# Optimization experiments

Hardware: AMD Instinct MI355X
Metric: run time of the kernel (lower is better)

Reference implementation:

```python
import jax, jax.numpy as jnp
import numpy as np

N_SRC0, N_DST0 = 100000, 20000   # block0: 100k src -> 20k dst
N_DST1 = 4096                    # block1: 20k src -> 4096 dst (seed nodes)


def setup_inputs() -> dict:
    key = jax.random.key(0)
    ks = jax.random.split(key, 8)
    E0, E1 = 640000, 131072
    return {
        "features": jax.random.normal(ks[0], (N_SRC0, 256), jnp.float32),
        "W1": jax.random.normal(ks[1], (256, 256), jnp.float32) * (1.0 / np.sqrt(256)),
        "b1": jnp.zeros((256,), jnp.float32),
        "W2": jax.random.normal(ks[2], (256, 128), jnp.float32) * (1.0 / np.sqrt(256)),
        "b2": jnp.zeros((128,), jnp.float32),
        "src0": jax.random.randint(ks[3], (E0,), 0, N_SRC0, jnp.int32),
        "dst0": jax.random.randint(ks[4], (E0,), 0, N_DST0, jnp.int32),
        "src1": jax.random.randint(ks[5], (E1,), 0, N_DST0, jnp.int32),
        "dst1": jax.random.randint(ks[6], (E1,), 0, N_DST1, jnp.int32),
    }


def _graph_conv(src, dst, n_dst, feat, W, b):
    # DGL GraphConv, norm='both': D_out^{-1/2} gather-sum D_in^{-1/2}, then WX+b.
    n_src = feat.shape[0]
    ones = jnp.ones(src.shape[0], feat.dtype)
    out_deg = jax.ops.segment_sum(ones, src, num_segments=n_src)
    norm_src = jnp.clip(out_deg, 1.0, None) ** -0.5          # [n_src]
    h = feat * norm_src[:, None]
    agg = jax.ops.segment_sum(h[src], dst, num_segments=n_dst)  # sparse SpMM
    in_deg = jax.ops.segment_sum(ones, dst, num_segments=n_dst)
    norm_dst = jnp.clip(in_deg, 1.0, None) ** -0.5           # [n_dst]
    return (agg * norm_dst[:, None]) @ W + b


def reference(features, W1, b1, W2, b2, src0, dst0, src1, dst1):
    x = jax.nn.relu(_graph_conv(src0, dst0, N_DST0, features, W1, b1))
    x = _graph_conv(src1, dst1, N_DST1, x, W2, b2)
    return x
```

## Files before the change

### kernel.cpp

```cpp
#include <hip/hip_runtime.h>
#include <hip/hip_bf16.h>

#define K_DIM 256
#define RSTRIDE 128
#define EPB 8192

#define G0_DB 625
#define G0_SB 256
#define G0_SW 392
#define G1_DB 128
#define G1_SB 64
#define G1_SW 313

#define NB_FIN (G0_DB + G1_DB + G0_SB + G1_SB)

typedef short bf16x8 __attribute__((ext_vector_type(8)));
typedef float f32x4 __attribute__((ext_vector_type(4)));

static __device__ __forceinline__ unsigned short f2bf(float x) {
    __hip_bfloat16 b = __float2bfloat16(x);
    return *reinterpret_cast<unsigned short*>(&b);
}
static __device__ __forceinline__ float bflo(unsigned int p) {
    return __uint_as_float(p << 16);
}
static __device__ __forceinline__ float bfhi(unsigned int p) {
    return __uint_as_float(p & 0xffff0000u);
}

static __device__ __forceinline__ void block_exscan(
        const int* __restrict__ hist, int* __restrict__ offs, int* __restrict__ tmp, int M) {
    const int tid = threadIdx.x;
    const int S = (M + 255) >> 8;
    const int base = tid * S;
    int sum = 0;
    for (int k = 0; k < S; ++k) {
        int idx = base + k;
        if (idx < M) sum += hist[idx];
    }
    tmp[tid] = sum;
    __syncthreads();
    for (int d = 1; d < 256; d <<= 1) {
        int v = tmp[tid];
        int u = (tid >= d) ? tmp[tid - d] : 0;
        __syncthreads();
        tmp[tid] = v + u;
        __syncthreads();
    }
    int run = (tid == 0) ? 0 : tmp[tid - 1];
    for (int k = 0; k < S; ++k) {
        int idx = base + k;
        if (idx < M) { offs[idx] = run; run += hist[idx]; }
    }
    __syncthreads();
}

struct SplitSh {
    int hist[640];
    int offs[640];
    int tmp[256];
    unsigned sorted[EPB];
};

template <int NDB, int NSB, int SW>
static __device__ __forceinline__ void split_sort(
        const int* __restrict__ src, const int* __restrict__ dst, int E, int chunk,
        int* __restrict__ cntD, int* __restrict__ offD,
        int* __restrict__ cntS, int* __restrict__ offS,
        unsigned* __restrict__ sortD, unsigned* __restrict__ sortS, SplitSh& sh) {
    const int tid = threadIdx.x;
    const int e0 = chunk * EPB;
    const int n = min(EPB, E - e0);
    for (int i = tid; i < NDB; i += 256) sh.hist[i] = 0;
    __syncthreads();
    for (int j = tid; j < n; j += 256) atomicAdd(&sh.hist[dst[e0 + j] >> 5], 1);
    __syncthreads();
    block_exscan(sh.hist, sh.offs, sh.tmp, NDB);
    for (int i = tid; i < NDB; i += 256) {
        cntD[chunk * NDB + i] = sh.hist[i];
        offD[chunk * NDB + i] = sh.offs[i];
    }
    __syncthreads();
    for (int j = tid; j < n; j += 256) {
        int d = dst[e0 + j];
        int s = src[e0 + j];
        int pos = atomicAdd(&sh.offs[d >> 5], 1);
        sh.sorted[pos] = ((unsigned)s << 5) | (unsigned)(d & 31);
    }
    __syncthreads();
    {
        unsigned* __restrict__ gout = sortD + (size_t)chunk * EPB;
        for (int j = tid; j < n; j += 256) gout[j] = sh.sorted[j];
    }
    __syncthreads();
    for (int i = tid; i < NSB; i += 256) sh.hist[i] = 0;
    __syncthreads();
    for (int j = tid; j < n; j += 256)
        atomicAdd(&sh.hist[(int)((unsigned)src[e0 + j] / SW)], 1);
    __syncthreads();
    block_exscan(sh.hist, sh.offs, sh.tmp, NSB);
    for (int i = tid; i < NSB; i += 256) {
        cntS[chunk * NSB + i] = sh.hist[i];
        offS[chunk * NSB + i] = sh.offs[i];
    }
    __syncthreads();
    for (int j = tid; j < n; j += 256) {
        unsigned s = (unsigned)src[e0 + j];
        int pos = atomicAdd(&sh.offs[s / SW], 1);
        sh.sorted[pos] = s;
    }
    __syncthreads();
    {
        unsigned* __restrict__ gout = sortS + (size_t)chunk * EPB;
        for (int j = tid; j < n; j += 256) gout[j] = sh.sorted[j];
    }
}

__global__ __launch_bounds__(256) void splitA_kernel(
        const int* __restrict__ src0, const int* __restrict__ dst0, int E0,
        const int* __restrict__ src1, const int* __restrict__ dst1, int E1,
        int* __restrict__ cntD0, int* __restrict__ offD0,
        int* __restrict__ cntS0, int* __restrict__ offS0,
        unsigned* __restrict__ sortD0, unsigned* __restrict__ sortS0,
        int* __restrict__ cntD1, int* __restrict__ offD1,
        int* __restrict__ cntS1, int* __restrict__ offS1,
        unsigned* __restrict__ sortD1, unsigned* __restrict__ sortS1,
        int nA0, int nA1,
        const float* __restrict__ feat, unsigned short* __restrict__ h, int total_f,
        int castBlocks,
        const float* __restrict__ W1, uint4* __restrict__ pw1,
        const float* __restrict__ W2, uint4* __restrict__ pw2) {
    __shared__ SplitSh sh;
    const int b = blockIdx.x;
    if (b < nA0) {
        split_sort<G0_DB, G0_SB, G0_SW>(src0, dst0, E0, b,
                                        cntD0, offD0, cntS0, offS0, sortD0, sortS0, sh);
    } else if (b < nA0 + nA1) {
        split_sort<G1_DB, G1_SB, G1_SW>(src1, dst1, E1, b - nA0,
                                        cntD1, offD1, cntS1, offS1, sortD1, sortS1, sh);
    } else if (b < nA0 + nA1 + castBlocks) {
        int idx = ((b - nA0 - nA1) * blockDim.x + threadIdx.x) * 8;
        if (idx >= total_f) return;
        const float4 v0 = *reinterpret_cast<const float4*>(feat + idx);
        const float4 v1 = *reinterpret_cast<const float4*>(feat + idx + 4);
        union { ushort4 u4[2]; uint4 u; } o;
        o.u4[0].x = f2bf(v0.x); o.u4[0].y = f2bf(v0.y);
        o.u4[0].z = f2bf(v0.z); o.u4[0].w = f2bf(v0.w);
        o.u4[1].x = f2bf(v1.x); o.u4[1].y = f2bf(v1.y);
        o.u4[1].z = f2bf(v1.z); o.u4[1].w = f2bf(v1.w);
        *reinterpret_cast<uint4*>(h + idx) = o.u;
    } else if (b < nA0 + nA1 + castBlocks + 32) {
        int idx = (b - nA0 - nA1 - castBlocks) * blockDim.x + threadIdx.x;
        int lane = idx & 63;
        int kt = (idx >> 6) & 7;
        int nt = idx >> 9;
        int n = nt * 16 + (lane & 15);
        int k = kt * 32 + (lane >> 4) * 8;
        union { unsigned short us[8]; uint4 u; } o;
#pragma unroll
        for (int j = 0; j < 8; ++j) o.us[j] = f2bf(W1[(size_t)(k + j) * 256 + n]);
        pw1[idx] = o.u;
    } else {
        int idx = (b - nA0 - nA1 - castBlocks - 32) * blockDim.x + threadIdx.x;
        int lane = idx & 63;
        int kt = (idx >> 6) & 7;
        int nt = idx >> 9;
        int n = nt * 16 + (lane & 15);
        int k = kt * 32 + (lane >> 4) * 8;
        union { unsigned short us[8]; uint4 u; } o;
#pragma unroll
        for (int j = 0; j < 8; ++j) o.us[j] = f2bf(W2[(size_t)(k + j) * 128 + n]);
        pw2[idx] = o.u;
    }
}

template <int NDB, int GT>
static __device__ __forceinline__ void fin_dst(
        const unsigned* __restrict__ sortD, const int* __restrict__ cntD,
        const int* __restrict__ offD, int nblk, int b,
        int* __restrict__ esrc, int* __restrict__ cnt, int* tile, int* rowc) {
    const int tid = threadIdx.x;
    if (tid < 32) rowc[tid] = 0;
    __syncthreads();
    for (int rr = tid / GT; rr < nblk; rr += 256 / GT) {
        const int c = cntD[rr * NDB + b];
        const int o = offD[rr * NDB + b];
        const unsigned* __restrict__ seg = sortD + (size_t)rr * EPB + o;
        for (int j = tid % GT; j < c; j += GT) {
            unsigned v = seg[j];
            int dloc = v & 31;
            int s = (int)(v >> 5);
            int slot = atomicAdd(&rowc[dloc], 1);
            if (slot < RSTRIDE) tile[(dloc << 7) + slot] = s;
        }
    }
    __syncthreads();
    int* __restrict__ gout = esrc + ((size_t)b << 12);
    for (int i = tid; i < 32 * RSTRIDE; i += 256) gout[i] = tile[i];
    if (tid < 32) cnt[b * 32 + tid] = rowc[tid];
}

template <int NSB, int SW, int GT>
static __device__ __forceinline__ void fin_src(
        const unsigned* __restrict__ sortS, const int* __restrict__ cntS,
        const int* __restrict__ offS, int nblk, int b, int NN,
        float* __restrict__ nv, int* hist) {
    const int tid = threadIdx.x;
    for (int i = tid; i < SW; i += 256) hist[i] = 0;
    __syncthreads();
    const int base = b * SW;
    for (int rr = tid / GT; rr < nblk; rr += 256 / GT) {
        const int c = cntS[rr * NSB + b];
        const int o = offS[rr * NSB + b];
        const unsigned* __restrict__ seg = sortS + (size_t)rr * EPB + o;
        for (int j = tid % GT; j < c; j += GT)
            atomicAdd(&hist[(int)seg[j] - base], 1);
    }
    __syncthreads();
    for (int i = tid; i < SW; i += 256) {
        int node = base + i;
        if (node < NN) nv[node] = rsqrtf((float)max(hist[i], 1));
    }
}

__global__ __launch_bounds__(256) void finalize_kernel(
        int nA0, int nA1,
        const unsigned* __restrict__ sortD0, const int* __restrict__ cntD0,
        const int* __restrict__ offD0, int* __restrict__ cnt0, int* __restrict__ esrc0,
        const unsigned* __restrict__ sortD1, const int* __restrict__ cntD1,
        const int* __restrict__ offD1, int* __restrict__ cnt1, int* __restrict__ esrc1,
        const unsigned* __restrict__ sortS0, const int* __restrict__ cntS0,
        const int* __restrict__ offS0, float* __restrict__ nv0,
        const unsigned* __restrict__ sortS1, const int* __restrict__ cntS1,
        const int* __restrict__ offS1, float* __restrict__ nv1) {
    __shared__ union {
        struct { int tile[32 * RSTRIDE]; int rowc[32]; } d;
        int hist[G0_SW];
    } sh;
    int b = blockIdx.x;
    if (b < G0_DB) {
        fin_dst<G0_DB, 2>(sortD0, cntD0, offD0, nA0, b, esrc0, cnt0, sh.d.tile, sh.d.rowc);
    } else if (b < G0_DB + G1_DB) {
        fin_dst<G1_DB, 16>(sortD1, cntD1, offD1, nA1, b - G0_DB, esrc1, cnt1,
                           sh.d.tile, sh.d.rowc);
    } else if (b < G0_DB + G1_DB + G0_SB) {
        fin_src<G0_SB, G0_SW, 2>(sortS0, cntS0, offS0, nA0, b - G0_DB - G1_DB,
                                 100000, nv0, sh.hist);
    } else {
        fin_src<G1_SB, G1_SW, 16>(sortS1, cntS1, offS1, nA1, b - G0_DB - G1_DB - G0_SB,
                                  20000, nv1, sh.hist);
    }
}

template <bool NORM>
static __device__ __forceinline__ void gather2_to_lds(
        const unsigned short* __restrict__ hfeat, const int* __restrict__ esrc,
        const int* __restrict__ cnt, const float* __restrict__ nv,
        int m0, int w, int lane, unsigned short (*Alds)[264]) {
#pragma unroll
    for (int k = 0; k < 2; ++k) {
        const int rloc = w * 2 + k;
        const int row = m0 + rloc;
        const int c = cnt[row];
        const int cend = min(c, RSTRIDE);
        const int* __restrict__ ep = esrc + ((size_t)row << 7);
        float a0 = 0.f, a1 = 0.f, a2 = 0.f, a3 = 0.f;
        int i = 0;
        for (; i + 7 < cend; i += 8) {
            int s[8];
            uint2 p[8];
            float nn[8];
#pragma unroll
            for (int u = 0; u < 8; ++u) s[u] = ep[i + u];
#pragma unroll
            for (int u = 0; u < 8; ++u)
                p[u] = *reinterpret_cast<const uint2*>(hfeat + (((size_t)s[u]) << 8) + lane * 4);
#pragma unroll
            for (int u = 0; u < 8; ++u)
                nn[u] = NORM ? nv[s[u]] : 1.0f;
#pragma unroll
            for (int u = 0; u < 8; ++u) {
                if (NORM) {
                    a0 = fmaf(bflo(p[u].x), nn[u], a0); a1 = fmaf(bfhi(p[u].x), nn[u], a1);
                    a2 = fmaf(bflo(p[u].y), nn[u], a2); a3 = fmaf(bfhi(p[u].y), nn[u], a3);
                } else {
                    a0 += bflo(p[u].x); a1 += bfhi(p[u].x);
                    a2 += bflo(p[u].y); a3 += bfhi(p[u].y);
                }
            }
        }
        for (; i < cend; ++i) {
            int s0 = ep[i];
            float n0 = NORM ? nv[s0] : 1.0f;
            const uint2 p0 = *reinterpret_cast<const uint2*>(hfeat + (((size_t)s0) << 8) + lane * 4);
            if (NORM) {
                a0 = fmaf(bflo(p0.x), n0, a0); a1 = fmaf(bfhi(p0.x), n0, a1);
                a2 = fmaf(bflo(p0.y), n0, a2); a3 = fmaf(bfhi(p0.y), n0, a3);
            } else {
                a0 += bflo(p0.x); a1 += bfhi(p0.x);
                a2 += bflo(p0.y); a3 += bfhi(p0.y);
            }
        }
        float nd = rsqrtf((float)max(c, 1));
        ushort4 o;
        o.x = f2bf(a0 * nd);
        o.y = f2bf(a1 * nd);
        o.z = f2bf(a2 * nd);
        o.w = f2bf(a3 * nd);
        *reinterpret_cast<ushort4*>(&Alds[rloc][lane * 4]) = o;
    }
}

__global__ __launch_bounds__(512, 8) void fused0_kernel(
        const unsigned short* __restrict__ hfeat, const int* __restrict__ esrc,
        const int* __restrict__ cnt, const float* __restrict__ nv0,
        const uint4* __restrict__ pW, const float* __restrict__ bias,
        const float* __restrict__ nv1, unsigned short* __restrict__ out) {
    __shared__ unsigned short Alds[16][264];
    const int m0 = blockIdx.x * 16;
    const int w = threadIdx.x >> 6;
    const int lane = threadIdx.x & 63;
    gather2_to_lds<true>(hfeat, esrc, cnt, nv0, m0, w, lane, Alds);
    __syncthreads();

    bf16x8 a[8];
    const unsigned short* ap = &Alds[lane & 15][(lane >> 4) * 8];
#pragma unroll
    for (int kt = 0; kt < 8; ++kt)
        a[kt] = *reinterpret_cast<const bf16x8*>(ap + kt * 32);

    const int rbase = m0 + (lane >> 4) * 4;
    float nsv[4];
#pragma unroll
    for (int r = 0; r < 4; ++r) nsv[r] = nv1[rbase + r];

#pragma unroll
    for (int nt = 0; nt < 2; ++nt) {
        const int n0 = w * 32 + nt * 16;
        f32x4 acc = {0.f, 0.f, 0.f, 0.f};
#pragma unroll
        for (int kt = 0; kt < 8; ++kt) {
            bf16x8 b = *reinterpret_cast<const bf16x8*>(&pW[((size_t)(n0 >> 4) * 8 + kt) * 64 + lane]);
            acc = __builtin_amdgcn_mfma_f32_16x16x32_bf16(a[kt], b, acc, 0, 0, 0);
        }
        const int col = n0 + (lane & 15);
        const float bv = bias[col];
#pragma unroll
        for (int r = 0; r < 4; ++r) {
            float v = fmaxf(acc[r] + bv, 0.0f) * nsv[r];
            out[(size_t)(rbase + r) * K_DIM + col] = f2bf(v);
        }
    }
}

__global__ __launch_bounds__(512, 8) void fused1_kernel(
        const unsigned short* __restrict__ xb, const int* __restrict__ esrc,
        const int* __restrict__ cnt,
        const uint4* __restrict__ pW, const float* __restrict__ bias,
        float* __restrict__ out) {
    __shared__ unsigned short Alds[16][264];
    const int m0 = blockIdx.x * 16;
    const int w = threadIdx.x >> 6;
    const int lane = threadIdx.x & 63;
    gather2_to_lds<false>(xb, esrc, cnt, nullptr, m0, w, lane, Alds);
    __syncthreads();

    bf16x8 a[8];
    const unsigned short* ap = &Alds[lane & 15][(lane >> 4) * 8];
#pragma unroll
    for (int kt = 0; kt < 8; ++kt)
        a[kt] = *reinterpret_cast<const bf16x8*>(ap + kt * 32);

    const int rbase = m0 + (lane >> 4) * 4;
    {
        const int n0 = w * 16;
        f32x4 acc = {0.f, 0.f, 0.f, 0.f};
#pragma unroll
        for (int kt = 0; kt < 8; ++kt) {
            bf16x8 b = *reinterpret_cast<const bf16x8*>(&pW[((size_t)(n0 >> 4) * 8 + kt) * 64 + lane]);
            acc = __builtin_amdgcn_mfma_f32_16x16x32_bf16(a[kt], b, acc, 0, 0, 0);
        }
        const int col = n0 + (lane & 15);
        const float bv = bias[col];
#pragma unroll
        for (int r = 0; r < 4; ++r)
            out[(size_t)(rbase + r) * 128 + col] = acc[r] + bv;
    }
}

__global__ __launch_bounds__(256) void gatherf_kernel(
        const float* __restrict__ feat, const int* __restrict__ esrc,
        const int* __restrict__ cnt, const int* __restrict__ od,
        float* __restrict__ outbuf, int n_dst) {
    int row = blockIdx.x * (blockDim.x >> 6) + (threadIdx.x >> 6);
    int lane = threadIdx.x & 63;
    if (row >= n_dst) return;
    const int c = cnt[row];
    const int cend = min(c, RSTRIDE);
    const int* __restrict__ ep = esrc + ((size_t)row << 7);
    float4 acc = {0.f, 0.f, 0.f, 0.f};
    for (int i = 0; i < cend; ++i) {
        int s0 = ep[i];
        float n0 = rsqrtf((float)max(od[s0], 1));
        const float4 v0 = *reinterpret_cast<const float4*>(feat + (((size_t)s0) << 8) + lane * 4);
        acc.x = fmaf(v0.x, n0, acc.x); acc.y = fmaf(v0.y, n0, acc.y);
        acc.z = fmaf(v0.z, n0, acc.z); acc.w = fmaf(v0.w, n0, acc.w);
    }
    float nd = rsqrtf((float)max(c, 1));
    float4 o = {acc.x * nd, acc.y * nd, acc.z * nd, acc.w * nd};
    *reinterpret_cast<float4*>(outbuf + (((size_t)row) << 8) + lane * 4) = o;
}

__global__ void edges_kernel(const int* __restrict__ src0, const int* __restrict__ dst0,
                             int* __restrict__ od0, int* __restrict__ cnt0,
                             int* __restrict__ esrc0, int E0,
                             const int* __restrict__ src1, const int* __restrict__ dst1,
                             int* __restrict__ od1, int* __restrict__ cnt1,
                             int* __restrict__ esrc1, int E1) {
    int i = blockIdx.x * blockDim.x + threadIdx.x;
    if (i < E0) {
        int s = src0[i];
        int d = dst0[i];
        atomicAdd(&od0[s], 1);
        int slot = atomicAdd(&cnt0[d], 1);
        if (slot < RSTRIDE) esrc0[(d << 7) + slot] = s;
    } else if (i < E0 + E1) {
        int e = i - E0;
        int s = src1[e];
        int d = dst1[e];
        atomicAdd(&od1[s], 1);
        int slot = atomicAdd(&cnt1[d], 1);
        if (slot < RSTRIDE) esrc1[(d << 7) + slot] = s;
    }
}

template <int ROWS, int NCOLS, bool RELU>
__global__ __launch_bounds__(NCOLS) void gemm_kernel(
        const float* __restrict__ A, const float* __restrict__ W,
        const float* __restrict__ bias, float* __restrict__ out, int M) {
    const int row0 = blockIdx.x * ROWS;
    const int c = threadIdx.x;
    const float* __restrict__ Ablk = A + (size_t)row0 * K_DIM;
    const float* __restrict__ Wc = W + c;

    float acc[ROWS];
#pragma unroll
    for (int r = 0; r < ROWS; ++r) acc[r] = 0.0f;

    float w0 = Wc[0];
    float w1 = Wc[NCOLS];
    float w2 = Wc[2 * NCOLS];
    float w3 = Wc[3 * NCOLS];

#pragma unroll 2
    for (int k = 0; k < K_DIM - 4; k += 4) {
        const float* p = Wc + (size_t)(k + 4) * NCOLS;
        float n0 = p[0];
        float n1 = p[NCOLS];
        float n2 = p[2 * NCOLS];
        float n3 = p[3 * NCOLS];
#pragma unroll
        for (int r = 0; r < ROWS; ++r) {
            const float4 a = *reinterpret_cast<const float4*>(Ablk + r * K_DIM + k);
            acc[r] = fmaf(a.x, w0, acc[r]);
            acc[r] = fmaf(a.y, w1, acc[r]);
            acc[r] = fmaf(a.z, w2, acc[r]);
            acc[r] = fmaf(a.w, w3, acc[r]);
        }
        w0 = n0; w1 = n1; w2 = n2; w3 = n3;
    }
    {
        const int k = K_DIM - 4;
#pragma unroll
        for (int r = 0; r < ROWS; ++r) {
            const float4 a = *reinterpret_cast<const float4*>(Ablk + r * K_DIM + k);
            acc[r] = fmaf(a.x, w0, acc[r]);
            acc[r] = fmaf(a.y, w1, acc[r]);
            acc[r] = fmaf(a.z, w2, acc[r]);
            acc[r] = fmaf(a.w, w3, acc[r]);
        }
    }

    const float b = bias[c];
#pragma unroll
    for (int r = 0; r < ROWS; ++r) {
        float v = acc[r] + b;
        if (RELU) v = fmaxf(v, 0.0f);
        out[(size_t)(row0 + r) * NCOLS + c] = v;
    }
}

extern "C" void kernel_launch(void* const* d_in, const int* in_sizes, int n_in,
                              void* d_out, int out_size, void* d_ws, size_t ws_size,
                              hipStream_t stream) {
    const float* features = (const float*)d_in[0];
    const float* W1 = (const float*)d_in[1];
    const float* b1 = (const float*)d_in[2];
    const float* W2 = (const float*)d_in[3];
    const float* b2 = (const float*)d_in[4];
    const int* src0 = (const int*)d_in[5];
    const int* dst0 = (const int*)d_in[6];
    const int* src1 = (const int*)d_in[7];
    const int* dst1 = (const int*)d_in[8];
    const int E0 = in_sizes[5];
    const int E1 = in_sizes[7];
    const int NSRC0 = 100000, NDST0 = 20000, NDST1 = 4096;
    const int nA0 = (E0 + EPB - 1) / EPB;
    const int nA1 = (E1 + EPB - 1) / EPB;

    char* ws = (char*)d_ws;
    size_t off = 0;
    auto carve = [&](size_t bytes) -> void* {
        void* p = ws + off;
        off = (off + bytes + 255) & ~(size_t)255;
        return p;
    };
    int* od0  = (int*)carve((size_t)NSRC0 * 4);
    int* od1  = (int*)carve((size_t)NDST0 * 4);
    int* cnt0 = (int*)carve((size_t)NDST0 * 4);
    int* cnt1 = (int*)carve((size_t)NDST1 * 4);
    const size_t zero_span = off;
    int* esrc0p = (int*)carve((size_t)NDST0 * RSTRIDE * 4);
    int* esrc1p = (int*)carve((size_t)NDST1 * RSTRIDE * 4);
    uint4* pW1  = (uint4*)carve((size_t)8192 * 16);
    uint4* pW2  = (uint4*)carve((size_t)4096 * 16);
    int* cntD0 = (int*)carve((size_t)nA0 * G0_DB * 4);
    int* offD0 = (int*)carve((size_t)nA0 * G0_DB * 4);
    int* cntS0 = (int*)carve((size_t)nA0 * G0_SB * 4);
    int* offS0 = (int*)carve((size_t)nA0 * G0_SB * 4);
    int* cntD1 = (int*)carve((size_t)nA1 * G1_DB * 4);
    int* offD1 = (int*)carve((size_t)nA1 * G1_DB * 4);
    int* cntS1 = (int*)carve((size_t)nA1 * G1_SB * 4);
    int* offS1 = (int*)carve((size_t)nA1 * G1_SB * 4);
    unsigned* sortD0 = (unsigned*)carve((size_t)nA0 * EPB * 4);
    unsigned* sortS0 = (unsigned*)carve((size_t)nA0 * EPB * 4);
    unsigned* sortD1 = (unsigned*)carve((size_t)nA1 * EPB * 4);
    unsigned* sortS1 = (unsigned*)carve((size_t)nA1 * EPB * 4);
    unsigned short* xbufb = (unsigned short*)carve((size_t)NDST0 * K_DIM * 2);
    unsigned short* hfeat = (unsigned short*)carve((size_t)NSRC0 * K_DIM * 2);
    const size_t need_bf16 = off;
    (void)n_in; (void)out_size;

    if (ws_size >= need_bf16) {
        float* nv0 = (float*)od0;
        float* nv1 = (float*)od1;
        const int total_f = NSRC0 * K_DIM;
        const int castBlocks = (total_f / 8 + 255) / 256;
        splitA_kernel<<<nA0 + nA1 + castBlocks + 48, 256, 0, stream>>>(
            src0, dst0, E0, src1, dst1, E1,
            cntD0, offD0, cntS0, offS0, sortD0, sortS0,
            cntD1, offD1, cntS1, offS1, sortD1, sortS1,
            nA0, nA1, features, hfeat, total_f, castBlocks,
            W1, pW1, W2, pW2);
        finalize_kernel<<<NB_FIN, 256, 0, stream>>>(
            nA0, nA1,
            sortD0, cntD0, offD0, cnt0, esrc0p,
            sortD1, cntD1, offD1, cnt1, esrc1p,
            sortS0, cntS0, offS0, nv0,
            sortS1, cntS1, offS1, nv1);
        fused0_kernel<<<NDST0 / 16, 512, 0, stream>>>(
            hfeat, esrc0p, cnt0, nv0, pW1, b1, nv1, xbufb);
        fused1_kernel<<<NDST1 / 16, 512, 0, stream>>>(
            xbufb, esrc1p, cnt1, pW2, b2, (float*)d_out);
    } else {
        hipMemsetAsync(ws, 0, zero_span, stream);
        float* agg0 = (float*)carve((size_t)NDST0 * K_DIM * 4);
        float* xbuf = (float*)carve((size_t)NDST0 * K_DIM * 4);
        float* agg1 = (float*)carve((size_t)NDST1 * K_DIM * 4);
        edges_kernel<<<(E0 + E1 + 255) / 256, 256, 0, stream>>>(
            src0, dst0, od0, cnt0, esrc0p, E0,
            src1, dst1, od1, cnt1, esrc1p, E1);
        gatherf_kernel<<<(NDST0 + 3) / 4, 256, 0, stream>>>(features, esrc0p, cnt0, od0,
                                                            agg0, NDST0);
        gemm_kernel<16, 256, true><<<NDST0 / 16, 256, 0, stream>>>(agg0, W1, b1, xbuf, NDST0);
        gatherf_kernel<<<(NDST1 + 3) / 4, 256, 0, stream>>>(xbuf, esrc1p, cnt1, od1,
                                                            agg1, NDST1);
        gemm_kernel<4, 128, false><<<NDST1 / 4, 128, 0, stream>>>(agg1, W2, b2,
                                                                  (float*)d_out, NDST1);
    }
}
```

Baseline: 279.7 us.

## Bucket per-row edge lists by source range for gather locality; halve edges-per-block

```diff
diff --git a/kernel.cpp b/kernel.cpp
--- a/kernel.cpp
+++ b/kernel.cpp
@@ -3,14 +3,16 @@
 
 #define K_DIM 256
 #define RSTRIDE 128
-#define EPB 8192
+#define EPB 4096
 
 #define G0_DB 625
 #define G0_SB 256
 #define G0_SW 392
+#define G0_GDIV 12500
 #define G1_DB 128
 #define G1_SB 64
 #define G1_SW 313
+#define G1_GDIV 2500
 
 #define NB_FIN (G0_DB + G1_DB + G0_SB + G1_SB)
 
@@ -174,13 +176,35 @@
     }
 }
 
-template <int NDB, int GT>
+template <int NDB, int GT, int GDIV>
 static __device__ __forceinline__ void fin_dst(
         const unsigned* __restrict__ sortD, const int* __restrict__ cntD,
         const int* __restrict__ offD, int nblk, int b,
-        int* __restrict__ esrc, int* __restrict__ cnt, int* tile, int* rowc) {
+        int* __restrict__ esrc, int* __restrict__ cnt,
+        int* tile, int* gcur, int* gtot) {
     const int tid = threadIdx.x;
-    if (tid < 32) rowc[tid] = 0;
+    for (int i = tid; i < 256; i += 256) gcur[i] = 0;
+    __syncthreads();
+    for (int rr = tid / GT; rr < nblk; rr += 256 / GT) {
+        const int c = cntD[rr * NDB + b];
+        const int o = offD[rr * NDB + b];
+        const unsigned* __restrict__ seg = sortD + (size_t)rr * EPB + o;
+        for (int j = tid % GT; j < c; j += GT) {
+            unsigned v = seg[j];
+            atomicAdd(&gcur[((v & 31) << 3) + (int)((v >> 5) / GDIV)], 1);
+        }
+    }
+    __syncthreads();
+    if (tid < 32) {
+        int run = 0;
+#pragma unroll
+        for (int g = 0; g < 8; ++g) {
+            int hh = gcur[(tid << 3) + g];
+            gcur[(tid << 3) + g] = run;
+            run += hh;
+        }
+        gtot[tid] = run;
+    }
     __syncthreads();
     for (int rr = tid / GT; rr < nblk; rr += 256 / GT) {
         const int c = cntD[rr * NDB + b];
@@ -190,14 +214,14 @@
             unsigned v = seg[j];
             int dloc = v & 31;
             int s = (int)(v >> 5);
-            int slot = atomicAdd(&rowc[dloc], 1);
+            int slot = atomicAdd(&gcur[(dloc << 3) + (int)((unsigned)s / GDIV)], 1);
             if (slot < RSTRIDE) tile[(dloc << 7) + slot] = s;
         }
     }
     __syncthreads();
     int* __restrict__ gout = esrc + ((size_t)b << 12);
     for (int i = tid; i < 32 * RSTRIDE; i += 256) gout[i] = tile[i];
-    if (tid < 32) cnt[b * 32 + tid] = rowc[tid];
+    if (tid < 32) cnt[b * 32 + tid] = gtot[tid];
 }
 
 template <int NSB, int SW, int GT>
@@ -234,21 +258,22 @@
         const unsigned* __restrict__ sortS1, const int* __restrict__ cntS1,
         const int* __restrict__ offS1, float* __restrict__ nv1) {
     __shared__ union {
-        struct { int tile[32 * RSTRIDE]; int rowc[32]; } d;
+        struct { int tile[32 * RSTRIDE]; int gcur[256]; int gtot[32]; } d;
         int hist[G0_SW];
     } sh;
     int b = blockIdx.x;
     if (b < G0_DB) {
-        fin_dst<G0_DB, 2>(sortD0, cntD0, offD0, nA0, b, esrc0, cnt0, sh.d.tile, sh.d.rowc);
+        fin_dst<G0_DB, 2, G0_GDIV>(sortD0, cntD0, offD0, nA0, b, esrc0, cnt0,
+                                   sh.d.tile, sh.d.gcur, sh.d.gtot);
     } else if (b < G0_DB + G1_DB) {
-        fin_dst<G1_DB, 16>(sortD1, cntD1, offD1, nA1, b - G0_DB, esrc1, cnt1,
-                           sh.d.tile, sh.d.rowc);
+        fin_dst<G1_DB, 8, G1_GDIV>(sortD1, cntD1, offD1, nA1, b - G0_DB, esrc1, cnt1,
+                                   sh.d.tile, sh.d.gcur, sh.d.gtot);
     } else if (b < G0_DB + G1_DB + G0_SB) {
         fin_src<G0_SB, G0_SW, 2>(sortS0, cntS0, offS0, nA0, b - G0_DB - G1_DB,
                                  100000, nv0, sh.hist);
     } else {
-        fin_src<G1_SB, G1_SW, 16>(sortS1, cntS1, offS1, nA1, b - G0_DB - G1_DB - G0_SB,
-                                  20000, nv1, sh.hist);
+        fin_src<G1_SB, G1_SW, 8>(sortS1, cntS1, offS1, nA1, b - G0_DB - G1_DB - G0_SB,
+                                 20000, nv1, sh.hist);
     }
 }
 
```

Result: faster. 270.8 us (-3.2%).
